# Kernel optimization log

Measured on AMD Instinct MI355X. Metric: run time of the kernel, lower is better.

Reference implementation:

```python
import jax, jax.numpy as jnp
import numpy as np
import math

D_K = 64

def setup_inputs() -> dict:
    key = jax.random.key(0)
    k1, k2, k3, k4 = jax.random.split(key, 4)
    B, H, S, D = 2, 16, 2048, D_K
    query = jax.random.normal(k1, (B, H, S, D), dtype=jnp.float32)
    kk = jax.random.normal(k2, (B, H, S, D), dtype=jnp.float32)
    value = jax.random.normal(k3, (B, H, S, D), dtype=jnp.float32)
    mask = jax.random.randint(k4, (B, 1, S, S), 0, 2).astype(bool)
    return {"query": query, "key": kk, "value": value, "mask": mask}

def reference(query, key, value, mask):
    # score = Q K^T / sqrt(d_k)  -> [B,H,S,S]
    score = jnp.einsum('bhqd,bhkd->bhqk', query, key) * (1.0 / math.sqrt(D_K))
    # masked_fill(mask, -inf)
    score = jnp.where(mask, -jnp.inf, score)
    attn = jax.nn.softmax(score, axis=-1)
    # rows that are fully masked produce NaN -> 0 (torch.nan_to_num)
    attn = jnp.nan_to_num(attn, nan=0.0)
    # dropout with drop_rate=0 is identity
    return jnp.einsum('bhqk,bhkd->bhqd', attn, value)
```

## Files before the change

kernel.cpp:

```cpp
#include <hip/hip_runtime.h>
#include <hip/hip_bf16.h>


#define S_LEN 2048
#define D_DIM 64
#define BH    32
#define BM    64
#define BN    64
#define PST   72
#define QSCALE 0.1803368801f

typedef __bf16    bf16_t;
typedef _Float16  f16_t;
typedef bf16_t bf16x8 __attribute__((ext_vector_type(8)));
typedef f16_t  f16x4  __attribute__((ext_vector_type(4)));
typedef float  f32x4  __attribute__((ext_vector_type(4)));
typedef unsigned char  u8;
typedef unsigned long long u64b;

__device__ __forceinline__ void load_lds16(const void* g, void* l) {
    __builtin_amdgcn_global_load_lds(
        (const __attribute__((address_space(1))) void*)g,
        (__attribute__((address_space(3))) void*)l, 16, 0, 0);
}

__global__ __launch_bounds__(256)
void mask_to_bits(const unsigned* __restrict__ M, u64b* __restrict__ bm)
{
    const int t = threadIdx.x;
    unsigned p = M[(t * 8179) & ((1 << 21) - 1)];
    const int is_u8 = __syncthreads_or(p > 1u);
    const int id = blockIdx.x * 256 + t;
    u64b w = 0;
    if (is_u8) {
        const uint4* src = (const uint4*)((const u8*)M + (size_t)id * 64);
        #pragma unroll
        for (int g = 0; g < 4; ++g) {
            uint4 x = src[g];
            const unsigned dw[4] = {x.x, x.y, x.z, x.w};
            #pragma unroll
            for (int q = 0; q < 4; ++q) {
                const unsigned v = dw[q];
                const int base = g * 16 + q * 4;
                if (v & 0x000000FFu) w |= 1ull << (base + 0);
                if (v & 0x0000FF00u) w |= 1ull << (base + 1);
                if (v & 0x00FF0000u) w |= 1ull << (base + 2);
                if (v & 0xFF000000u) w |= 1ull << (base + 3);
            }
        }
    } else {
        const uint4* src = (const uint4*)(M + (size_t)id * 64);
        #pragma unroll
        for (int g = 0; g < 16; ++g) {
            uint4 x = src[g];
            if (x.x) w |= 1ull << (g * 4 + 0);
            if (x.y) w |= 1ull << (g * 4 + 1);
            if (x.z) w |= 1ull << (g * 4 + 2);
            if (x.w) w |= 1ull << (g * 4 + 3);
        }
    }
    bm[id] = w;
}

__global__ __launch_bounds__(256)
void k_prep(const float* __restrict__ K, bf16_t* __restrict__ Kb)
{
    const size_t i = ((size_t)blockIdx.x * 256 + threadIdx.x) * 8;
    float4 a = *(const float4*)(K + i);
    float4 b = *(const float4*)(K + i + 4);
    bf16x8 w;
    w[0]=(bf16_t)a.x; w[1]=(bf16_t)a.y; w[2]=(bf16_t)a.z; w[3]=(bf16_t)a.w;
    w[4]=(bf16_t)b.x; w[5]=(bf16_t)b.y; w[6]=(bf16_t)b.z; w[7]=(bf16_t)b.w;
    const size_t r = i >> 6;
    const int    g = (int)((i & 63) >> 3);
    *(bf16x8*)(Kb + r * 64 + ((g ^ (int)(r & 7)) * 8)) = w;
}

__global__ __launch_bounds__(256)
void v_transpose(const float* __restrict__ V, f16_t* __restrict__ Vt)
{
    __shared__ f16_t T[128][PST];
    const int t  = threadIdx.x;
    const int sc = blockIdx.x;
    const int bh = blockIdx.y;
    const float* Vh = V + ((size_t)bh * S_LEN + sc * 128) * D_DIM;
    #pragma unroll
    for (int it = 0; it < 4; ++it) {
        const int row = it * 32 + (t >> 3);
        const int c8  = (t & 7) * 8;
        float4 a = *(const float4*)(Vh + row * D_DIM + c8);
        float4 b = *(const float4*)(Vh + row * D_DIM + c8 + 4);
        f16_t* d = &T[row][c8];
        d[0]=(f16_t)a.x; d[1]=(f16_t)a.y; d[2]=(f16_t)a.z; d[3]=(f16_t)a.w;
        d[4]=(f16_t)b.x; d[5]=(f16_t)b.y; d[6]=(f16_t)b.z; d[7]=(f16_t)b.w;
    }
    __syncthreads();
    const int d = t >> 2;
    #pragma unroll
    for (int g = 0; g < 4; ++g) {
        const int s_off = (t & 3) * 32 + g * 8;
        const int kbt   = sc * 2 + (s_off >> 6);
        const int k_in  = s_off & 63;
        const int gk    = k_in >> 3;
        f16x4 w0, w1;
        #pragma unroll
        for (int j = 0; j < 4; ++j) { w0[j] = T[s_off + j][d]; w1[j] = T[s_off + 4 + j][d]; }
        f16_t* dst = Vt + (((size_t)bh * (S_LEN/BN) + kbt) * D_DIM + d) * 64
                        + ((gk ^ (d & 7)) * 8);
        *(f16x4*)dst = w0;
        *(f16x4*)(dst + 4) = w1;
    }
}

__global__ __launch_bounds__(256, 4)
void fa_fwd(const float* __restrict__ Q, const float* __restrict__ K,
            const float* __restrict__ V, const void* __restrict__ M,
            const u64b* __restrict__ bm, const bf16_t* __restrict__ Kb,
            const f16_t* __restrict__ Vt, float* __restrict__ O)
{
    __shared__ __align__(16) bf16_t KldsA[BN * D_DIM];
    __shared__ __align__(16) bf16_t KldsB[BN * D_DIM];
    __shared__ __align__(16) f16_t  VldsA[D_DIM * BN];
    __shared__ __align__(16) f16_t  VldsB[D_DIM * BN];

    const int tid  = threadIdx.x;
    const int wave = tid >> 6;
    const int lane = tid & 63;
    const int quad = lane >> 4;
    const int ln   = lane & 15;

    const int qt = blockIdx.x;
    const int bh = blockIdx.y;
    const int b  = bh >> 4;
    const int qbase = qt * BM + wave * 16;

    const size_t head_off = (size_t)bh * S_LEN * D_DIM;
    const float* Qh = Q + head_off;
    const float* Kh = K + head_off;
    const float* Vh = V + head_off;
    const bf16_t* Kbh = Kb ? (Kb + head_off) : nullptr;
    const u8*  Mb8  = (const u8*)M  + (size_t)b * S_LEN * S_LEN;
    const int* Mb32 = (const int*)M + (size_t)b * S_LEN * S_LEN;

    int mask_is_u8 = 0;
    if (!bm) {
        int probe = ((const int*)M)[(tid * 8179) & ((1 << 21) - 1)];
        mask_is_u8 = __syncthreads_or((unsigned)probe > 1u);
    }

    bf16x8 qfrag[2];
    {
        const float* qrow = Qh + (size_t)(qbase + ln) * D_DIM;
        #pragma unroll
        for (int s = 0; s < 2; ++s) {
            float4 a = *(const float4*)(qrow + s * 32 + quad * 8);
            float4 c = *(const float4*)(qrow + s * 32 + quad * 8 + 4);
            bf16x8 w;
            w[0]=(bf16_t)(a.x*QSCALE); w[1]=(bf16_t)(a.y*QSCALE);
            w[2]=(bf16_t)(a.z*QSCALE); w[3]=(bf16_t)(a.w*QSCALE);
            w[4]=(bf16_t)(c.x*QSCALE); w[5]=(bf16_t)(c.y*QSCALE);
            w[6]=(bf16_t)(c.z*QSCALE); w[7]=(bf16_t)(c.w*QSCALE);
            qfrag[s] = w;
        }
    }

    f32x4 accO[4] = {{0.f,0.f,0.f,0.f},{0.f,0.f,0.f,0.f},
                     {0.f,0.f,0.f,0.f},{0.f,0.f,0.f,0.f}};
    float lpart = 0.f;

    const int xg = ln & 7;
    const size_t bmrow = ((size_t)b * S_LEN + qbase + ln) * 32;

    auto load_wm = [&](int kb) -> u64b {
        if (bm) return bm[bmrow + (kb >> 6)];
        u64b w = 0;
        if (mask_is_u8) {
            const u8* mp = Mb8 + (size_t)(qbase + ln) * S_LEN + kb;
            #pragma unroll
            for (int t = 0; t < 4; ++t)
                #pragma unroll
                for (int j = 0; j < 4; ++j) {
                    const int k = t*16 + quad*4 + j;
                    if (mp[k]) w |= 1ull << k;
                }
        } else {
            const int* mp = Mb32 + (size_t)(qbase + ln) * S_LEN + kb;
            #pragma unroll
            for (int t = 0; t < 4; ++t)
                #pragma unroll
                for (int j = 0; j < 4; ++j) {
                    const int k = t*16 + quad*4 + j;
                    if (mp[k]) w |= 1ull << k;
                }
        }
        return w;
    };

    auto prefetch = [&](int kb, bf16_t* Kl, f16_t* Vl) {
        const bf16_t* kt = Kbh + (size_t)kb * D_DIM;
        const f16_t*  vt = Vt + ((size_t)bh * (S_LEN/BN) + (kb >> 6)) * (BN * D_DIM);
        #pragma unroll
        for (int i = 0; i < 2; ++i) {
            const int c = wave + 4 * i;
            load_lds16(kt + c * 512 + lane * 8, Kl + c * 512);
            load_lds16(vt + c * 512 + lane * 8, Vl + c * 512);
        }
    };

    auto compute_tile = [&](const bf16_t* Kl, const f16_t* Vl, u64b wm) {
        f32x4 St[4] = {{0.f,0.f,0.f,0.f},{0.f,0.f,0.f,0.f},
                       {0.f,0.f,0.f,0.f},{0.f,0.f,0.f,0.f}};
        #pragma unroll
        for (int s = 0; s < 2; ++s) {
            #pragma unroll
            for (int t = 0; t < 4; ++t) {
                bf16x8 ak = *(const bf16x8*)
                    &Kl[(16*t + ln) * D_DIM + (((s*4 + quad) ^ xg) * 8)];
                St[t] = __builtin_amdgcn_mfma_f32_16x16x32_bf16(ak, qfrag[s], St[t], 0, 0, 0);
            }
        }
        f16x4 pa[4];
        #pragma unroll
        for (int t = 0; t < 4; ++t) {
            const unsigned nib = (unsigned)(wm >> (t*16 + quad*4)) & 0xFu;
            #pragma unroll
            for (int j = 0; j < 4; ++j) {
                const float p = (nib & (1u << j)) ? 0.f
                              : __builtin_amdgcn_exp2f(St[t][j]);
                lpart += p;
                pa[t][j] = (f16_t)p;
            }
        }
        #pragma unroll
        for (int t = 0; t < 4; ++t) {
            #pragma unroll
            for (int dt = 0; dt < 4; ++dt) {
                const int g = 2*t + (quad >> 1);
                f16x4 bv = *(const f16x4*)
                    &Vl[(dt*16 + ln) * D_DIM + ((g ^ xg) * 8) + (quad & 1) * 4];
                accO[dt] = __builtin_amdgcn_mfma_f32_16x16x16f16(pa[t], bv, accO[dt], 0, 0, 0);
            }
        }
    };

    if (Kbh) {
        prefetch(0, KldsA, VldsA);
        for (int kb = 0; kb < S_LEN; kb += 2 * BN) {
            __syncthreads();
            u64b wm = load_wm(kb);
            if (kb + BN < S_LEN) prefetch(kb + BN, KldsB, VldsB);
            compute_tile(KldsA, VldsA, wm);
            __syncthreads();
            wm = load_wm(kb + BN);
            if (kb + 2*BN < S_LEN) prefetch(kb + 2*BN, KldsA, VldsA);
            compute_tile(KldsB, VldsB, wm);
        }
    } else {
        const int srow = tid >> 2;
        const int sgrp = tid & 3;
        for (int kb = 0; kb < S_LEN; kb += BN) {
            __syncthreads();
            const float* kp = Kh + (size_t)(kb + srow) * D_DIM + sgrp * 16;
            #pragma unroll
            for (int h = 0; h < 2; ++h) {
                float4 a = *(const float4*)(kp + h * 8);
                float4 c = *(const float4*)(kp + h * 8 + 4);
                bf16x8 w;
                w[0]=(bf16_t)a.x; w[1]=(bf16_t)a.y; w[2]=(bf16_t)a.z; w[3]=(bf16_t)a.w;
                w[4]=(bf16_t)c.x; w[5]=(bf16_t)c.y; w[6]=(bf16_t)c.z; w[7]=(bf16_t)c.w;
                const int g = sgrp * 2 + h;
                *(bf16x8*)&KldsA[srow * D_DIM + ((g ^ (srow & 7)) * 8)] = w;
            }
            const float* vp = Vh + (size_t)(kb + srow) * D_DIM + sgrp * 16;
            float vv[16];
            #pragma unroll
            for (int g = 0; g < 4; ++g) {
                float4 a = *(const float4*)(vp + g * 4);
                vv[g*4+0]=a.x; vv[g*4+1]=a.y; vv[g*4+2]=a.z; vv[g*4+3]=a.w;
            }
            const int gk = srow >> 3;
            #pragma unroll
            for (int jj = 0; jj < 16; ++jj) {
                const int j = (jj + srow) & 15;
                const int d = sgrp * 16 + j;
                VldsA[d * D_DIM + ((gk ^ (d & 7)) * 8) + (srow & 7)] = (f16_t)vv[j];
            }
            __syncthreads();
            compute_tile(KldsA, VldsA, load_wm(kb));
        }
    }

    lpart += __shfl_xor(lpart, 16, 64);
    lpart += __shfl_xor(lpart, 32, 64);
    #pragma unroll
    for (int r = 0; r < 4; ++r) {
        const float lr  = __shfl(lpart, quad * 4 + r, 64);
        const float inv = (lr > 0.f) ? 1.f / lr : 0.f;
        float* orow = O + head_off + (size_t)(qbase + quad*4 + r) * D_DIM;
        #pragma unroll
        for (int dt = 0; dt < 4; ++dt)
            orow[16*dt + ln] = accO[dt][r] * inv;
    }
}

extern "C" void kernel_launch(void* const* d_in, const int* in_sizes, int n_in,
                              void* d_out, int out_size, void* d_ws, size_t ws_size,
                              hipStream_t stream) {
    (void)in_sizes; (void)n_in; (void)out_size;
    const float* Q = (const float*)d_in[0];
    const float* K = (const float*)d_in[1];
    const float* V = (const float*)d_in[2];
    const void*  M = d_in[3];
    float* O = (float*)d_out;

    const size_t bm_bytes = (size_t)2 * S_LEN * (S_LEN / 64) * 8;
    const size_t kv_elems = (size_t)BH * S_LEN * D_DIM;
    const size_t need_all = bm_bytes + 2 * kv_elems * 2;

    u64b*   bm = (ws_size >= bm_bytes) ? (u64b*)d_ws : nullptr;
    bf16_t* Kb = nullptr; f16_t* Vt = nullptr;
    if (ws_size >= need_all) {
        Kb = (bf16_t*)((char*)d_ws + bm_bytes);
        Vt = (f16_t*)(Kb + kv_elems);
    }

    if (bm)
        mask_to_bits<<<dim3(131072 / 256), dim3(256), 0, stream>>>(
            (const unsigned*)M, bm);
    if (Kb) {
        k_prep<<<dim3((unsigned)(kv_elems / 8 / 256)), dim3(256), 0, stream>>>(K, Kb);
        v_transpose<<<dim3(S_LEN / 128, BH), dim3(256), 0, stream>>>(V, Vt);
    }

    dim3 grid(S_LEN / BM, BH);
    fa_fwd<<<grid, dim3(256), 0, stream>>>(Q, K, V, M, bm, Kb, Vt, O);
}
```

Baseline: 181.0 us.

## Switch attention tiles to 32x32 MFMA with split-K waves and LDS reduction

Replaces the 16x16 MFMA layout, where each wave handled 16 query rows over all 64 keys, with 32x32x16 bf16 and 32x32x8 f16 MFMAs. Waves now split the block into two query halves and two key halves of each tile. Each wave keeps partial O and row sums, and these are merged at the end through LDS. The V transpose layout is changed to match the new fragment order. The aim is higher MFMA throughput and fewer LDS fragment loads per FLOP, at the cost of an extra end-of-kernel reduction, a barrier, and possibly more register pressure.

```diff
diff --git a/kernel.cpp b/kernel.cpp
--- a/kernel.cpp
+++ b/kernel.cpp
@@ -14,7 +14,8 @@
 typedef _Float16  f16_t;
 typedef bf16_t bf16x8 __attribute__((ext_vector_type(8)));
 typedef f16_t  f16x4  __attribute__((ext_vector_type(4)));
-typedef float  f32x4  __attribute__((ext_vector_type(4)));
+typedef f16_t  f16x8  __attribute__((ext_vector_type(8)));
+typedef float  f32x16 __attribute__((ext_vector_type(16)));
 typedef unsigned char  u8;
 typedef unsigned long long u64b;
 
@@ -101,14 +102,15 @@
         const int s_off = (t & 3) * 32 + g * 8;
         const int kbt   = sc * 2 + (s_off >> 6);
         const int k_in  = s_off & 63;
-        const int gk    = k_in >> 3;
+        const int c     = k_in >> 3;
         f16x4 w0, w1;
         #pragma unroll
         for (int j = 0; j < 4; ++j) { w0[j] = T[s_off + j][d]; w1[j] = T[s_off + 4 + j][d]; }
-        f16_t* dst = Vt + (((size_t)bh * (S_LEN/BN) + kbt) * D_DIM + d) * 64
-                        + ((gk ^ (d & 7)) * 8);
-        *(f16x4*)dst = w0;
-        *(f16x4*)(dst + 4) = w1;
+        f16_t* row = Vt + (((size_t)bh * (S_LEN/BN) + kbt) * D_DIM + d) * 64;
+        const int g0 = (c >> 1) * 2;
+        const int sub = (c & 1) * 4;
+        *(f16x4*)(row + ((g0 ^ (d & 7)) * 8) + sub) = w0;
+        *(f16x4*)(row + (((g0+1) ^ (d & 7)) * 8) + sub) = w1;
     }
 }
 
@@ -126,13 +128,17 @@
     const int tid  = threadIdx.x;
     const int wave = tid >> 6;
     const int lane = tid & 63;
-    const int quad = lane >> 4;
-    const int ln   = lane & 15;
+    const int h    = lane >> 5;
+    const int n32  = lane & 31;
+
+    const int qh = wave & 1;
+    const int kh = wave >> 1;
 
     const int qt = blockIdx.x;
     const int bh = blockIdx.y;
     const int b  = bh >> 4;
-    const int qbase = qt * BM + wave * 16;
+    const int qbase = qt * BM;
+    const int qrow_g = qbase + qh * 32 + n32;
 
     const size_t head_off = (size_t)bh * S_LEN * D_DIM;
     const float* Qh = Q + head_off;
@@ -148,13 +154,14 @@
         mask_is_u8 = __syncthreads_or((unsigned)probe > 1u);
     }
 
-    bf16x8 qfrag[2];
+    bf16x8 qfrag[4];
     {
-        const float* qrow = Qh + (size_t)(qbase + ln) * D_DIM;
-        #pragma unroll
-        for (int s = 0; s < 2; ++s) {
-            float4 a = *(const float4*)(qrow + s * 32 + quad * 8);
-            float4 c = *(const float4*)(qrow + s * 32 + quad * 8 + 4);
+        const float* qrow = Qh + (size_t)qrow_g * D_DIM;
+        #pragma unroll
+        for (int s = 0; s < 4; ++s) {
+            const int d0 = s * 16 + h * 8;
+            float4 a = *(const float4*)(qrow + d0);
+            float4 c = *(const float4*)(qrow + d0 + 4);
             bf16x8 w;
             w[0]=(bf16_t)(a.x*QSCALE); w[1]=(bf16_t)(a.y*QSCALE);
             w[2]=(bf16_t)(a.z*QSCALE); w[3]=(bf16_t)(a.w*QSCALE);
@@ -164,34 +171,29 @@
         }
     }
 
-    f32x4 accO[4] = {{0.f,0.f,0.f,0.f},{0.f,0.f,0.f,0.f},
-                     {0.f,0.f,0.f,0.f},{0.f,0.f,0.f,0.f}};
+    f32x16 accO[2];
+    #pragma unroll
+    for (int dt = 0; dt < 2; ++dt)
+        #pragma unroll
+        for (int r = 0; r < 16; ++r) accO[dt][r] = 0.f;
     float lpart = 0.f;
 
-    const int xg = ln & 7;
-    const size_t bmrow = ((size_t)b * S_LEN + qbase + ln) * 32;
+    const int rowK = kh * 32 + n32;
+    const int xk = rowK & 7;
+    const int xv = n32 & 7;
+
+    const size_t bmrow = ((size_t)b * S_LEN + qrow_g) * 32;
 
     auto load_wm = [&](int kb) -> u64b {
         if (bm) return bm[bmrow + (kb >> 6)];
         u64b w = 0;
-        if (mask_is_u8) {
-            const u8* mp = Mb8 + (size_t)(qbase + ln) * S_LEN + kb;
-            #pragma unroll
-            for (int t = 0; t < 4; ++t)
-                #pragma unroll
-                for (int j = 0; j < 4; ++j) {
-                    const int k = t*16 + quad*4 + j;
-                    if (mp[k]) w |= 1ull << k;
-                }
-        } else {
-            const int* mp = Mb32 + (size_t)(qbase + ln) * S_LEN + kb;
-            #pragma unroll
-            for (int t = 0; t < 4; ++t)
-                #pragma unroll
-                for (int j = 0; j < 4; ++j) {
-                    const int k = t*16 + quad*4 + j;
-                    if (mp[k]) w |= 1ull << k;
-                }
+        #pragma unroll
+        for (int r = 0; r < 16; ++r) {
+            const int kl = kh*32 + (r & 3) + 8 * (r >> 2) + 4 * h;
+            const bool m = mask_is_u8
+                ? (Mb8 [(size_t)qrow_g * S_LEN + kb + kl] != 0)
+                : (Mb32[(size_t)qrow_g * S_LEN + kb + kl] != 0);
+            if (m) w |= 1ull << kl;
         }
         return w;
     };
@@ -208,37 +210,34 @@
     };
 
     auto compute_tile = [&](const bf16_t* Kl, const f16_t* Vl, u64b wm) {
-        f32x4 St[4] = {{0.f,0.f,0.f,0.f},{0.f,0.f,0.f,0.f},
-                       {0.f,0.f,0.f,0.f},{0.f,0.f,0.f,0.f}};
-        #pragma unroll
-        for (int s = 0; s < 2; ++s) {
-            #pragma unroll
-            for (int t = 0; t < 4; ++t) {
-                bf16x8 ak = *(const bf16x8*)
-                    &Kl[(16*t + ln) * D_DIM + (((s*4 + quad) ^ xg) * 8)];
-                St[t] = __builtin_amdgcn_mfma_f32_16x16x32_bf16(ak, qfrag[s], St[t], 0, 0, 0);
-            }
+        f32x16 St;
+        #pragma unroll
+        for (int r = 0; r < 16; ++r) St[r] = 0.f;
+        #pragma unroll
+        for (int s = 0; s < 4; ++s) {
+            bf16x8 kf = *(const bf16x8*)&Kl[rowK * 64 + (((2*s + h) ^ xk) * 8)];
+            St = __builtin_amdgcn_mfma_f32_32x32x16_bf16(kf, qfrag[s], St, 0, 0, 0);
         }
         f16x4 pa[4];
         #pragma unroll
-        for (int t = 0; t < 4; ++t) {
-            const unsigned nib = (unsigned)(wm >> (t*16 + quad*4)) & 0xFu;
-            #pragma unroll
-            for (int j = 0; j < 4; ++j) {
-                const float p = (nib & (1u << j)) ? 0.f
-                              : __builtin_amdgcn_exp2f(St[t][j]);
-                lpart += p;
-                pa[t][j] = (f16_t)p;
-            }
-        }
-        #pragma unroll
-        for (int t = 0; t < 4; ++t) {
-            #pragma unroll
-            for (int dt = 0; dt < 4; ++dt) {
-                const int g = 2*t + (quad >> 1);
-                f16x4 bv = *(const f16x4*)
-                    &Vl[(dt*16 + ln) * D_DIM + ((g ^ xg) * 8) + (quad & 1) * 4];
-                accO[dt] = __builtin_amdgcn_mfma_f32_16x16x16f16(pa[t], bv, accO[dt], 0, 0, 0);
+        for (int r = 0; r < 16; ++r) {
+            const int kl = kh*32 + (r & 3) + 8 * (r >> 2) + 4 * h;
+            const float p = ((wm >> kl) & 1ull) ? 0.f
+                          : __builtin_amdgcn_exp2f(St[r]);
+            lpart += p;
+            pa[r >> 2][r & 3] = (f16_t)p;
+        }
+        #pragma unroll
+        for (int cp2 = 0; cp2 < 2; ++cp2) {
+            const int cp = kh * 2 + cp2;
+            #pragma unroll
+            for (int dt = 0; dt < 2; ++dt) {
+                const f16_t* vr = &Vl[(dt*32 + n32) * 64 + (((cp*2 + h) ^ xv) * 8)];
+                f16x8 vv = *(const f16x8*)vr;
+                f16x4 v0 = __builtin_shufflevector(vv, vv, 0, 1, 2, 3);
+                f16x4 v1 = __builtin_shufflevector(vv, vv, 4, 5, 6, 7);
+                accO[dt] = __builtin_amdgcn_mfma_f32_32x32x8f16(pa[cp2*2+0], v0, accO[dt], 0, 0, 0);
+                accO[dt] = __builtin_amdgcn_mfma_f32_32x32x8f16(pa[cp2*2+1], v1, accO[dt], 0, 0, 0);
             }
         }
     };
@@ -262,14 +261,14 @@
             __syncthreads();
             const float* kp = Kh + (size_t)(kb + srow) * D_DIM + sgrp * 16;
             #pragma unroll
-            for (int h = 0; h < 2; ++h) {
-                float4 a = *(const float4*)(kp + h * 8);
-                float4 c = *(const float4*)(kp + h * 8 + 4);
+            for (int hh = 0; hh < 2; ++hh) {
+                float4 a = *(const float4*)(kp + hh * 8);
+                float4 c = *(const float4*)(kp + hh * 8 + 4);
                 bf16x8 w;
                 w[0]=(bf16_t)a.x; w[1]=(bf16_t)a.y; w[2]=(bf16_t)a.z; w[3]=(bf16_t)a.w;
                 w[4]=(bf16_t)c.x; w[5]=(bf16_t)c.y; w[6]=(bf16_t)c.z; w[7]=(bf16_t)c.w;
-                const int g = sgrp * 2 + h;
-                *(bf16x8*)&KldsA[srow * D_DIM + ((g ^ (srow & 7)) * 8)] = w;
+                const int g = sgrp * 2 + hh;
+                *(bf16x8*)&KldsA[srow * 64 + ((g ^ (srow & 7)) * 8)] = w;
             }
             const float* vp = Vh + (size_t)(kb + srow) * D_DIM + sgrp * 16;
             float vv[16];
@@ -278,28 +277,48 @@
                 float4 a = *(const float4*)(vp + g * 4);
                 vv[g*4+0]=a.x; vv[g*4+1]=a.y; vv[g*4+2]=a.z; vv[g*4+3]=a.w;
             }
-            const int gk = srow >> 3;
-            #pragma unroll
-            for (int jj = 0; jj < 16; ++jj) {
-                const int j = (jj + srow) & 15;
-                const int d = sgrp * 16 + j;
-                VldsA[d * D_DIM + ((gk ^ (d & 7)) * 8) + (srow & 7)] = (f16_t)vv[j];
+            const int c   = srow >> 3;
+            const int grp = (c >> 1) * 2 + ((srow >> 2) & 1);
+            const int sub = (c & 1) * 4 + (srow & 3);
+            #pragma unroll
+            for (int j16 = 0; j16 < 16; ++j16) {
+                const int d = sgrp * 16 + j16;
+                VldsA[d * 64 + ((grp ^ (d & 7)) * 8) + sub] = (f16_t)vv[j16];
             }
             __syncthreads();
             compute_tile(KldsA, VldsA, load_wm(kb));
         }
     }
 
-    lpart += __shfl_xor(lpart, 16, 64);
     lpart += __shfl_xor(lpart, 32, 64);
-    #pragma unroll
-    for (int r = 0; r < 4; ++r) {
-        const float lr  = __shfl(lpart, quad * 4 + r, 64);
-        const float inv = (lr > 0.f) ? 1.f / lr : 0.f;
-        float* orow = O + head_off + (size_t)(qbase + quad*4 + r) * D_DIM;
-        #pragma unroll
-        for (int dt = 0; dt < 4; ++dt)
-            orow[16*dt + ln] = accO[dt][r] * inv;
+    __syncthreads();
+    float* Vf = qh ? (float*)VldsB : (float*)VldsA;
+    float* Lf = (float*)KldsA;
+    if (kh == 1) {
+        #pragma unroll
+        for (int r = 0; r < 16; ++r) {
+            const int ql = (r & 3) + 8 * (r >> 2) + 4 * h;
+            #pragma unroll
+            for (int dt = 0; dt < 2; ++dt)
+                Vf[ql * 64 + dt * 32 + n32] = accO[dt][r];
+        }
+        if (lane < 32) Lf[qh * 32 + lane] = lpart;
+    }
+    __syncthreads();
+    if (kh == 0) {
+        const float lt  = lpart + Lf[qh * 32 + n32];
+        const float inv = (lt > 0.f) ? 1.f / lt : 0.f;
+        float* obase = O + head_off + (size_t)(qbase + qh * 32) * D_DIM;
+        #pragma unroll
+        for (int r = 0; r < 16; ++r) {
+            const int ql = (r & 3) + 8 * (r >> 2) + 4 * h;
+            const float inv_r = __shfl(inv, ql, 64);
+            #pragma unroll
+            for (int dt = 0; dt < 2; ++dt) {
+                const float o = (accO[dt][r] + Vf[ql * 64 + dt * 32 + n32]) * inv_r;
+                obase[(size_t)ql * D_DIM + dt * 32 + n32] = o;
+            }
+        }
     }
 }
 
```

Result: slower. 209.7 us (+15.8%).
